# Optimization experiments

Measured on AMD Instinct MI355X. Metric: run time of the kernel, lower is better.

Reference implementation:

```python
import jax, jax.numpy as jnp
import numpy as np

N = 50000
E = 800000
IN_FEATS = 256
N_HIDDEN = 64
N_CLASSES = 40
HEADS = (4, 1)
NEG_SLOPE = 0.2  # DGL GATConv default


def gat_layer(x, src, dst, W, attn_l, attn_r, bias, n_heads, out_dim, activation):
    """One dglnn.GATConv layer (eval mode: dropout disabled).

    x: [N, F_in]; src/dst: [E] edge endpoints; W: [F_in, H*D];
    attn_l/attn_r: [H, D]; bias: [H*D]. Returns [N, H, D].
    """
    n = x.shape[0]
    z = (x @ W).reshape(n, n_heads, out_dim)            # [N, H, D]
    el = jnp.sum(z * attn_l[None], axis=-1)            # [N, H]
    er = jnp.sum(z * attn_r[None], axis=-1)            # [N, H]
    e = jax.nn.leaky_relu(el[src] + er[dst], NEG_SLOPE)  # [E, H]
    # segment softmax over incoming edges of each dst node
    m = jax.ops.segment_max(e, dst, num_segments=n)     # [N, H]
    a = jnp.exp(e - m[dst])                             # [E, H]
    s = jax.ops.segment_sum(a, dst, num_segments=n)     # [N, H]
    alpha = a / s[dst]                                  # [E, H]
    msg = alpha[:, :, None] * z[src]                    # [E, H, D]
    out = jax.ops.segment_sum(msg, dst, num_segments=n)  # [N, H, D]
    out = out + bias.reshape(1, n_heads, out_dim)
    if activation is not None:
        out = activation(out)
    return out


def setup_inputs() -> dict:
    key = jax.random.key(0)
    ks = jax.random.split(key, 12)
    H0, H1 = HEADS
    d_in1 = N_HIDDEN * H0
    def glorot(k, shape):
        fan = sum(shape[:2]) if len(shape) > 1 else shape[0]
        return jax.random.normal(k, shape, jnp.float32) * (2.0 / fan) ** 0.5
    return {
        "x": jax.random.normal(ks[0], (N, IN_FEATS), jnp.float32),
        "src": jax.random.randint(ks[1], (E,), 0, N),
        "dst": jax.random.randint(ks[2], (E,), 0, N),
        "W0": glorot(ks[3], (IN_FEATS, H0 * N_HIDDEN)),
        "attn_l0": glorot(ks[4], (H0, N_HIDDEN)),
        "attn_r0": glorot(ks[5], (H0, N_HIDDEN)),
        "bias0": jnp.zeros((H0 * N_HIDDEN,), jnp.float32),
        "W1": glorot(ks[6], (d_in1, H1 * N_CLASSES)),
        "attn_l1": glorot(ks[7], (H1, N_CLASSES)),
        "attn_r1": glorot(ks[8], (H1, N_CLASSES)),
        "bias1": jnp.zeros((H1 * N_CLASSES,), jnp.float32),
    }


def reference(x, src, dst, W0, attn_l0, attn_r0, bias0, W1, attn_l1, attn_r1, bias1):
    H0, H1 = HEADS
    # layer 0: GATConv + ELU, then flatten heads (l==0 branch)
    h = gat_layer(x, src, dst, W0, attn_l0, attn_r0, bias0,
                  H0, N_HIDDEN, jax.nn.elu)              # [N, H0, D]
    h = h.reshape(h.shape[0], -1)                        # [N, H0*D]
    # layer 1 (last): GATConv, no activation, head-mean (l==1 branch)
    h = gat_layer(h, src, dst, W1, attn_l1, attn_r1, bias1,
                  H1, N_CLASSES, None)                   # [N, H1, C]
    return h.mean(axis=1)                                # [N, C]
```

## Files before the change

kernel.cpp:

```cpp
#include <hip/hip_runtime.h>
#include <math.h>

using bf16x8 = __attribute__((ext_vector_type(8))) short;
using f32x4  = __attribute__((ext_vector_type(4))) float;

__device__ __forceinline__ unsigned short f2bf(float v) {
  unsigned int b = __float_as_uint(v);
  unsigned int r = (b + 0x7fffu + ((b >> 16) & 1u)) >> 16;
  return (unsigned short)r;
}
__device__ __forceinline__ float bf2f(unsigned short u) {
  return __uint_as_float(((unsigned int)u) << 16);
}


__global__ void mega0_kernel(const float* __restrict__ W0f, unsigned short* __restrict__ Bp0,
                             const float* __restrict__ W1f, unsigned short* __restrict__ Bp1,
                             const int* __restrict__ dst, int* __restrict__ deg, int E) {
  int bx = blockIdx.x;
  if (bx >= 38) {
    int t = (bx - 38) * 256 + threadIdx.x;
    if (t < E) atomicAdd(&deg[dst[t]], 1);
    return;
  }
  int idx = bx * 256 + threadIdx.x;
  if (idx < 8192) {
    int lane = idx & 63, s = (idx >> 6) & 7, t = idx >> 9;
    int n = t * 16 + (lane & 15), quad = lane >> 4;
    unsigned short* o = Bp0 + (size_t)idx * 8;
    #pragma unroll
    for (int j = 0; j < 8; ++j) {
      int k = s * 32 + quad * 8 + j;
      o[j] = f2bf(W0f[(size_t)k * 256 + n]);
    }
  } else if (idx < 8192 + 1536) {
    int i1 = idx - 8192;
    int lane = i1 & 63, s = (i1 >> 6) & 7, t = i1 >> 9;
    int n = t * 16 + (lane & 15), quad = lane >> 4;
    unsigned short* o = Bp1 + (size_t)i1 * 8;
    #pragma unroll
    for (int j = 0; j < 8; ++j) {
      int k = s * 32 + quad * 8 + j;
      o[j] = (n < 40) ? f2bf(W1f[(size_t)k * 40 + n]) : 0;
    }
  }
}


__global__ void block_sum_kernel(const int* __restrict__ deg, int* __restrict__ bsum, int n) {
  __shared__ int red[4];
  int t = threadIdx.x, i = blockIdx.x * 256 + t;
  int v = (i < n) ? deg[i] : 0;
  #pragma unroll
  for (int off = 32; off; off >>= 1) v += __shfl_xor(v, off);
  if ((t & 63) == 0) red[t >> 6] = v;
  __syncthreads();
  if (t == 0) bsum[blockIdx.x] = red[0] + red[1] + red[2] + red[3];
}

__global__ void scan_bsum_kernel(const int* __restrict__ bsum, int* __restrict__ boffs,
                                 int* __restrict__ offsets, int nb, int n) {
  __shared__ int tmp[1024];
  int t = threadIdx.x;
  int v = (t < nb) ? bsum[t] : 0;
  tmp[t] = v;
  __syncthreads();
  #pragma unroll
  for (int off = 1; off < 1024; off <<= 1) {
    int add = (t >= off) ? tmp[t - off] : 0;
    __syncthreads();
    tmp[t] += add;
    __syncthreads();
  }
  if (t < nb) boffs[t] = tmp[t] - v;
  if (t == 1023) offsets[n] = tmp[1023];
}

__global__ void write_offsets_kernel(const int* __restrict__ deg, const int* __restrict__ boffs,
                                     int* __restrict__ offsets, int* __restrict__ cursor, int n) {
  __shared__ int tmp[256];
  int t = threadIdx.x, i = blockIdx.x * 256 + t;
  int v = (i < n) ? deg[i] : 0;
  tmp[t] = v;
  __syncthreads();
  #pragma unroll
  for (int off = 1; off < 256; off <<= 1) {
    int add = (t >= off) ? tmp[t - off] : 0;
    __syncthreads();
    tmp[t] += add;
    __syncthreads();
  }
  if (i < n) {
    int o = boffs[blockIdx.x] + tmp[t] - v;
    offsets[i] = o;
    cursor[i] = o;
  }
}


__global__ __launch_bounds__(512) void mega2_kernel(
    const float* __restrict__ A, const unsigned short* __restrict__ Bp,
    unsigned short* __restrict__ Zb,
    const float* __restrict__ al, const float* __restrict__ arr,
    float* __restrict__ el, float* __restrict__ er, int M,
    const int* __restrict__ src, const int* __restrict__ dst,
    int* __restrict__ cursor, int* __restrict__ ssrc, int E, int nG, int nC) {
  __shared__ unsigned short Bs[32768];
  int bx = blockIdx.x;
  int tid = threadIdx.x;

  if (bx >= nG) {
    int stride = nC * 512;
    for (int e = (bx - nG) * 512 + tid; e < E; e += stride) {
      int p = atomicAdd(&cursor[dst[e]], 1);
      ssrc[p] = src[e];
    }
    return;
  }

  int gx = bx >> 1, y = bx & 1;
  {
    const int4* s4 = (const int4*)(Bp + (size_t)y * 32768);
    int4* d4 = (int4*)Bs;
    #pragma unroll
    for (int i = 0; i < 8; ++i) d4[tid + i * 512] = s4[tid + i * 512];
  }
  __syncthreads();

  int wid = tid >> 6, lane = tid & 63;
  int quad = lane >> 4, col16 = lane & 15;
  int wr = wid >> 1, wc = wid & 1;
  int rowbase = gx * 256 + wr * 64;

  const float* aptr[4];
  #pragma unroll
  for (int rt = 0; rt < 4; ++rt) {
    int m = rowbase + rt * 16 + col16;
    if (m > M - 1) m = M - 1;
    aptr[rt] = A + (size_t)m * 256 + quad * 8;
  }

  f32x4 acc[4][4];
  #pragma unroll
  for (int rt = 0; rt < 4; ++rt)
    #pragma unroll
    for (int ct = 0; ct < 4; ++ct) acc[rt][ct] = {0.f, 0.f, 0.f, 0.f};

  const bf16x8* BsV = (const bf16x8*)Bs;

  auto loadA = [&](bf16x8* fr, int s) {
    #pragma unroll
    for (int rt = 0; rt < 4; ++rt) {
      const float* ap = aptr[rt] + s * 32;
      float4 a0 = *(const float4*)ap;
      float4 a1 = *(const float4*)(ap + 4);
      fr[rt][0] = (short)f2bf(a0.x); fr[rt][1] = (short)f2bf(a0.y);
      fr[rt][2] = (short)f2bf(a0.z); fr[rt][3] = (short)f2bf(a0.w);
      fr[rt][4] = (short)f2bf(a1.x); fr[rt][5] = (short)f2bf(a1.y);
      fr[rt][6] = (short)f2bf(a1.z); fr[rt][7] = (short)f2bf(a1.w);
    }
  };

  bf16x8 afc[4];
  loadA(afc, 0);
  for (int s = 0; s < 8; ++s) {
    bf16x8 afn[4];
    if (s < 7) loadA(afn, s + 1);
    #pragma unroll
    for (int ct = 0; ct < 4; ++ct) {
      bf16x8 bf = BsV[((wc * 4 + ct) * 8 + s) * 64 + lane];
      #pragma unroll
      for (int rt = 0; rt < 4; ++rt)
        acc[rt][ct] = __builtin_amdgcn_mfma_f32_16x16x32_bf16(afc[rt], bf, acc[rt][ct], 0, 0, 0);
    }
    if (s < 7) {
      #pragma unroll
      for (int rt = 0; rt < 4; ++rt) afc[rt] = afn[rt];
    }
  }

  int hw = y * 2 + wc;
  float al_c[4], ar_c[4];
  #pragma unroll
  for (int ct = 0; ct < 4; ++ct) {
    int col = y * 128 + (wc * 4 + ct) * 16 + col16;
    al_c[ct] = al[col];
    ar_c[ct] = arr[col];
  }

  #pragma unroll
  for (int rt = 0; rt < 4; ++rt) {
    int row0 = rowbase + rt * 16 + quad * 4;
    #pragma unroll
    for (int r = 0; r < 4; ++r) {
      int row = row0 + r;
      if (row < M) {
        #pragma unroll
        for (int ct = 0; ct < 4; ++ct) {
          int col = y * 128 + (wc * 4 + ct) * 16 + col16;
          Zb[(size_t)row * 256 + col] = f2bf(acc[rt][ct][r]);
        }
      }
      float pe = 0.f, pr = 0.f;
      #pragma unroll
      for (int ct = 0; ct < 4; ++ct) {
        float zv = acc[rt][ct][r];
        pe += zv * al_c[ct];
        pr += zv * ar_c[ct];
      }
      pe += __shfl_xor(pe, 1); pr += __shfl_xor(pr, 1);
      pe += __shfl_xor(pe, 2); pr += __shfl_xor(pr, 2);
      pe += __shfl_xor(pe, 4); pr += __shfl_xor(pr, 4);
      pe += __shfl_xor(pe, 8); pr += __shfl_xor(pr, 8);
      if (col16 == 0 && row < M) {
        el[(size_t)row * 4 + hw] = pe;
        er[(size_t)row * 4 + hw] = pr;
      }
    }
  }
}


__global__ __launch_bounds__(256) void gemm1_mfma_kernel(
    const unsigned short* __restrict__ Ab, const unsigned short* __restrict__ Bp,
    unsigned short* __restrict__ Zb,
    const float* __restrict__ al, const float* __restrict__ arr,
    float* __restrict__ el, float* __restrict__ er, int M) {
  int wid = threadIdx.x >> 6, lane = threadIdx.x & 63;
  int quad = lane >> 4, col16 = lane & 15;
  int m = blockIdx.x * 64 + wid * 16 + col16;

  f32x4 acc[3];
  #pragma unroll
  for (int t = 0; t < 3; ++t) acc[t] = {0.f, 0.f, 0.f, 0.f};

  const bf16x8* BpV = (const bf16x8*)Bp;

  for (int s = 0; s < 8; ++s) {
    bf16x8 af;
    if (m < M) {
      af = *(const bf16x8*)(Ab + (size_t)m * 256 + s * 32 + quad * 8);
    } else {
      #pragma unroll
      for (int j = 0; j < 8; ++j) af[j] = 0;
    }
    #pragma unroll
    for (int t = 0; t < 3; ++t) {
      bf16x8 bf = BpV[(t * 8 + s) * 64 + lane];
      acc[t] = __builtin_amdgcn_mfma_f32_16x16x32_bf16(af, bf, acc[t], 0, 0, 0);
    }
  }

  float al_c[3], ar_c[3];
  #pragma unroll
  for (int t = 0; t < 3; ++t) {
    int col = t * 16 + col16;
    al_c[t] = (col < 40) ? al[col] : 0.f;
    ar_c[t] = (col < 40) ? arr[col] : 0.f;
  }

  int row0 = blockIdx.x * 64 + wid * 16 + quad * 4;
  #pragma unroll
  for (int r = 0; r < 4; ++r) {
    int row = row0 + r;
    if (row < M) {
      #pragma unroll
      for (int t = 0; t < 3; ++t) {
        int col = t * 16 + col16;
        if (col < 40) Zb[(size_t)row * 40 + col] = f2bf(acc[t][r]);
      }
    }
    float pe = 0.f, pr = 0.f;
    #pragma unroll
    for (int t = 0; t < 3; ++t) {
      pe += acc[t][r] * al_c[t];
      pr += acc[t][r] * ar_c[t];
    }
    pe += __shfl_xor(pe, 1); pr += __shfl_xor(pr, 1);
    pe += __shfl_xor(pe, 2); pr += __shfl_xor(pr, 2);
    pe += __shfl_xor(pe, 4); pr += __shfl_xor(pr, 4);
    pe += __shfl_xor(pe, 8); pr += __shfl_xor(pr, 8);
    if (col16 == 0 && row < M) {
      el[row] = pe;
      er[row] = pr;
    }
  }
}


__global__ __launch_bounds__(256) void agg0_kernel(
    const int* __restrict__ offs, const int* __restrict__ ssrc,
    const float* __restrict__ el, const float* __restrict__ er,
    const unsigned short* __restrict__ zb, const float* __restrict__ bias,
    unsigned short* __restrict__ outb, int n) {
  __shared__ float sW[4][16][4];
  __shared__ int   sS[4][16];
  int wid  = threadIdx.x >> 6;
  int lane = threadIdx.x & 63;
  int node = blockIdx.x * 4 + wid;
  if (node >= n) return;
  int c = lane & 3, eoff = lane >> 2;
  int half = lane >> 5, colg = lane & 31, h2 = colg >> 3;
  int s0 = offs[node], s1 = offs[node + 1];
  float er_c = er[node * 4 + c];

  float ssum = 0.f;
  float acc[8] = {0.f, 0.f, 0.f, 0.f, 0.f, 0.f, 0.f, 0.f};
  for (int base = s0; base < s1; base += 16) {
    int cnt = min(16, s1 - base);
    if (eoff < cnt) {
      int esrc = ssrc[base + eoff];
      float v = el[esrc * 4 + c] + er_c;
      v = v > 0.f ? v : 0.2f * v;
      sW[wid][eoff][c] = expf(v);
      if (c == 0) sS[wid][eoff] = esrc;
    }
    for (int j = 0; j < cnt; j += 2) {
      int jj = j + half;
      float w = (jj < cnt) ? sW[wid][jj][h2] : 0.f;
      int sn = sS[wid][(jj < cnt) ? jj : (cnt - 1)];
      ssum += w;
      bf16x8 zu = *(const bf16x8*)(zb + (size_t)sn * 256 + (colg << 3));
      #pragma unroll
      for (int i = 0; i < 8; ++i)
        acc[i] += w * bf2f((unsigned short)zu[i]);
    }
  }

  ssum += __shfl_xor(ssum, 32);
  #pragma unroll
  for (int i = 0; i < 8; ++i) acc[i] += __shfl_xor(acc[i], 32);

  float inv = (s1 > s0) ? 1.f / ssum : 0.f;
  if (half == 0) {
    const float4 b0v = *(const float4*)(bias + (colg << 3));
    const float4 b1v = *(const float4*)(bias + (colg << 3) + 4);
    float bb[8] = {b0v.x, b0v.y, b0v.z, b0v.w, b1v.x, b1v.y, b1v.z, b1v.w};
    bf16x8 u;
    #pragma unroll
    for (int i = 0; i < 8; ++i) {
      float o = acc[i] * inv + bb[i];
      o = o > 0.f ? o : expm1f(o);
      u[i] = (short)f2bf(o);
    }
    *(bf16x8*)(outb + (size_t)node * 256 + (colg << 3)) = u;
  }
}


__global__ __launch_bounds__(256) void agg1_kernel(
    const int* __restrict__ offs, const int* __restrict__ ssrc,
    const float* __restrict__ el, const float* __restrict__ er,
    const unsigned short* __restrict__ zb, const float* __restrict__ bias,
    float* __restrict__ out, int n) {
  __shared__ float sW[4][64];
  __shared__ int   sS[4][64];
  int wid  = threadIdx.x >> 6;
  int lane = threadIdx.x & 63;
  int node = blockIdx.x * 4 + wid;
  if (node >= n) return;
  int half = lane >> 5, d = lane & 31;
  int s0 = offs[node], s1 = offs[node + 1];
  float ern = er[node];

  float ssum = 0.f;
  float2 acc = make_float2(0.f, 0.f);
  for (int base = s0; base < s1; base += 64) {
    int cnt = min(64, s1 - base);
    if (lane < cnt) {
      int esrc = ssrc[base + lane];
      float v = el[esrc] + ern;
      v = v > 0.f ? v : 0.2f * v;
      sW[wid][lane] = expf(v);
      sS[wid][lane] = esrc;
    }
    for (int j = 0; j < cnt; j += 2) {
      int jj = j + half;
      float w = (jj < cnt) ? sW[wid][jj] : 0.f;
      int sn = sS[wid][(jj < cnt) ? jj : (cnt - 1)];
      ssum += w;
      if (d < 20) {
        unsigned zp = *(const unsigned*)(zb + (size_t)sn * 40 + (d << 1));
        acc.x += w * bf2f((unsigned short)(zp & 0xffffu));
        acc.y += w * bf2f((unsigned short)(zp >> 16));
      }
    }
  }

  ssum  += __shfl_xor(ssum, 32);
  acc.x += __shfl_xor(acc.x, 32);
  acc.y += __shfl_xor(acc.y, 32);

  float inv = (s1 > s0) ? 1.f / ssum : 0.f;
  if (half == 0 && d < 20) {
    float2 o;
    o.x = acc.x * inv + bias[(d << 1) + 0];
    o.y = acc.y * inv + bias[(d << 1) + 1];
    *(float2*)(out + (size_t)node * 40 + (d << 1)) = o;
  }
}


extern "C" void kernel_launch(void* const* d_in, const int* in_sizes, int n_in,
                              void* d_out, int out_size, void* d_ws, size_t ws_size,
                              hipStream_t stream) {
  const float* x   = (const float*)d_in[0];
  const int*   src = (const int*)d_in[1];
  const int*   dst = (const int*)d_in[2];
  const float* W0  = (const float*)d_in[3];
  const float* al0 = (const float*)d_in[4];
  const float* ar0 = (const float*)d_in[5];
  const float* b0  = (const float*)d_in[6];
  const float* W1  = (const float*)d_in[7];
  const float* al1 = (const float*)d_in[8];
  const float* ar1 = (const float*)d_in[9];
  const float* b1  = (const float*)d_in[10];
  float* out = (float*)d_out;

  const int N = in_sizes[0] / 256;
  const int E = in_sizes[1];
  const int NB = (N + 255) / 256;

  char* ws = (char*)d_ws;
  size_t off = 0;
  auto alloc = [&](size_t bytes) {
    void* p = ws + off;
    off = (off + bytes + 255) & ~(size_t)255;
    return p;
  };
  unsigned short* z0b = (unsigned short*)alloc((size_t)N * 256 * 2);
  unsigned short* h0b = (unsigned short*)alloc((size_t)N * 256 * 2);
  unsigned short* z1b = (unsigned short*)alloc((size_t)N * 40 * 2);
  unsigned short* w0p = (unsigned short*)alloc((size_t)16 * 8 * 64 * 8 * 2);
  unsigned short* w1p = (unsigned short*)alloc((size_t)3 * 8 * 64 * 8 * 2);
  float* el0  = (float*)alloc((size_t)N * 4 * 4);
  float* er0  = (float*)alloc((size_t)N * 4 * 4);
  float* el1  = (float*)alloc((size_t)N * 4);
  float* er1  = (float*)alloc((size_t)N * 4);
  int* deg    = (int*)alloc((size_t)N * 4);
  int* offs   = (int*)alloc((size_t)(N + 1) * 4);
  int* cursor = (int*)alloc((size_t)N * 4);
  int* bsum   = (int*)alloc((size_t)NB * 4);
  int* boffs  = (int*)alloc((size_t)NB * 4);
  int* ssrc   = (int*)alloc((size_t)E * 4);
  (void)off; (void)ws_size; (void)n_in; (void)out_size;

  const int nG = ((N + 255) / 256) * 2;
  const int nH = (E + 255) / 256;
  const int nC = 391;

  hipMemsetAsync(deg, 0, (size_t)N * 4, stream);
  mega0_kernel<<<38 + nH, 256, 0, stream>>>(W0, w0p, W1, w1p, dst, deg, E);
  block_sum_kernel<<<NB, 256, 0, stream>>>(deg, bsum, N);
  scan_bsum_kernel<<<1, 1024, 0, stream>>>(bsum, boffs, offs, NB, N);
  write_offsets_kernel<<<NB, 256, 0, stream>>>(deg, boffs, offs, cursor, N);
  mega2_kernel<<<nG + nC, 512, 0, stream>>>(x, w0p, z0b, al0, ar0, el0, er0, N,
                                            src, dst, cursor, ssrc, E, nG, nC);
  agg0_kernel<<<(N + 3) / 4, 256, 0, stream>>>(offs, ssrc, el0, er0, z0b, b0, h0b, N);
  gemm1_mfma_kernel<<<(N + 63) / 64, 256, 0, stream>>>(h0b, w1p, z1b, al1, ar1, el1, er1, N);
  agg1_kernel<<<(N + 3) / 4, 256, 0, stream>>>(offs, ssrc, el1, er1, z1b, b1, out, N);
}
```

Before: 318.0 us.

## Pre-convert x to bf16 in setup kernel and feed GEMM bf16 directly

Adds a bf16 conversion pass for x into the first setup kernel, writing into the h0b buffer, so the layer-0 GEMM reads half-width bf16 A tiles instead of converting fp32 on the fly. The GEMM also issues its first A load before staging the weights into LDS and fully unrolls the k loop. This adds an extra full read of x plus a write of its bf16 copy, in exchange for halving A traffic and removing conversion ALU work inside each of the two column-tile blocks that read the same rows. It relies on h0b not being used until agg0 overwrites it.

```diff
diff --git a/kernel.cpp b/kernel.cpp
--- a/kernel.cpp
+++ b/kernel.cpp
@@ -16,11 +16,27 @@
 
 __global__ void mega0_kernel(const float* __restrict__ W0f, unsigned short* __restrict__ Bp0,
                              const float* __restrict__ W1f, unsigned short* __restrict__ Bp1,
-                             const int* __restrict__ dst, int* __restrict__ deg, int E) {
+                             const float* __restrict__ xf, unsigned short* __restrict__ xb,
+                             const int* __restrict__ dst, int* __restrict__ deg,
+                             int E, int nCV, size_t NT) {
   int bx = blockIdx.x;
+  if (bx >= 38 + nCV) {
+    int t = (bx - 38 - nCV) * 256 + threadIdx.x;
+    if (t < E) atomicAdd(&deg[dst[t]], 1);
+    return;
+  }
   if (bx >= 38) {
-    int t = (bx - 38) * 256 + threadIdx.x;
-    if (t < E) atomicAdd(&deg[dst[t]], 1);
+    size_t i = ((size_t)(bx - 38) * 256 + threadIdx.x) * 8;
+    if (i + 8 <= NT) {
+      float4 a0 = *(const float4*)(xf + i);
+      float4 a1 = *(const float4*)(xf + i + 4);
+      bf16x8 u;
+      u[0] = (short)f2bf(a0.x); u[1] = (short)f2bf(a0.y);
+      u[2] = (short)f2bf(a0.z); u[3] = (short)f2bf(a0.w);
+      u[4] = (short)f2bf(a1.x); u[5] = (short)f2bf(a1.y);
+      u[6] = (short)f2bf(a1.z); u[7] = (short)f2bf(a1.w);
+      *(bf16x8*)(xb + i) = u;
+    }
     return;
   }
   int idx = bx * 256 + threadIdx.x;
@@ -99,7 +115,7 @@
 
 
 __global__ __launch_bounds__(512) void mega2_kernel(
-    const float* __restrict__ A, const unsigned short* __restrict__ Bp,
+    const unsigned short* __restrict__ Ab, const unsigned short* __restrict__ Bp,
     unsigned short* __restrict__ Zb,
     const float* __restrict__ al, const float* __restrict__ arr,
     float* __restrict__ el, float* __restrict__ er, int M,
@@ -119,50 +135,45 @@
   }
 
   int gx = bx >> 1, y = bx & 1;
-  {
-    const int4* s4 = (const int4*)(Bp + (size_t)y * 32768);
-    int4* d4 = (int4*)Bs;
-    #pragma unroll
-    for (int i = 0; i < 8; ++i) d4[tid + i * 512] = s4[tid + i * 512];
-  }
-  __syncthreads();
-
   int wid = tid >> 6, lane = tid & 63;
   int quad = lane >> 4, col16 = lane & 15;
   int wr = wid >> 1, wc = wid & 1;
   int rowbase = gx * 256 + wr * 64;
 
-  const float* aptr[4];
+  const unsigned short* aptr[4];
   #pragma unroll
   for (int rt = 0; rt < 4; ++rt) {
     int m = rowbase + rt * 16 + col16;
     if (m > M - 1) m = M - 1;
-    aptr[rt] = A + (size_t)m * 256 + quad * 8;
-  }
-
-  f32x4 acc[4][4];
-  #pragma unroll
-  for (int rt = 0; rt < 4; ++rt)
-    #pragma unroll
-    for (int ct = 0; ct < 4; ++ct) acc[rt][ct] = {0.f, 0.f, 0.f, 0.f};
-
-  const bf16x8* BsV = (const bf16x8*)Bs;
+    aptr[rt] = Ab + (size_t)m * 256 + quad * 8;
+  }
 
   auto loadA = [&](bf16x8* fr, int s) {
     #pragma unroll
-    for (int rt = 0; rt < 4; ++rt) {
-      const float* ap = aptr[rt] + s * 32;
-      float4 a0 = *(const float4*)ap;
-      float4 a1 = *(const float4*)(ap + 4);
-      fr[rt][0] = (short)f2bf(a0.x); fr[rt][1] = (short)f2bf(a0.y);
-      fr[rt][2] = (short)f2bf(a0.z); fr[rt][3] = (short)f2bf(a0.w);
-      fr[rt][4] = (short)f2bf(a1.x); fr[rt][5] = (short)f2bf(a1.y);
-      fr[rt][6] = (short)f2bf(a1.z); fr[rt][7] = (short)f2bf(a1.w);
-    }
+    for (int rt = 0; rt < 4; ++rt)
+      fr[rt] = *(const bf16x8*)(aptr[rt] + s * 32);
   };
 
   bf16x8 afc[4];
   loadA(afc, 0);
+
+  {
+    const int4* s4 = (const int4*)(Bp + (size_t)y * 32768);
+    int4* d4 = (int4*)Bs;
+    #pragma unroll
+    for (int i = 0; i < 8; ++i) d4[tid + i * 512] = s4[tid + i * 512];
+  }
+  __syncthreads();
+
+  f32x4 acc[4][4];
+  #pragma unroll
+  for (int rt = 0; rt < 4; ++rt)
+    #pragma unroll
+    for (int ct = 0; ct < 4; ++ct) acc[rt][ct] = {0.f, 0.f, 0.f, 0.f};
+
+  const bf16x8* BsV = (const bf16x8*)Bs;
+
+  #pragma unroll
   for (int s = 0; s < 8; ++s) {
     bf16x8 afn[4];
     if (s < 7) loadA(afn, s + 1);
@@ -445,16 +456,20 @@
   int* ssrc   = (int*)alloc((size_t)E * 4);
   (void)off; (void)ws_size; (void)n_in; (void)out_size;
 
+  unsigned short* xb = h0b;
+  const size_t NT = (size_t)N * 256;
+  const int nCV = (int)((NT / 8 + 255) / 256);
+
   const int nG = ((N + 255) / 256) * 2;
   const int nH = (E + 255) / 256;
   const int nC = 391;
 
   hipMemsetAsync(deg, 0, (size_t)N * 4, stream);
-  mega0_kernel<<<38 + nH, 256, 0, stream>>>(W0, w0p, W1, w1p, dst, deg, E);
+  mega0_kernel<<<38 + nCV + nH, 256, 0, stream>>>(W0, w0p, W1, w1p, x, xb, dst, deg, E, nCV, NT);
   block_sum_kernel<<<NB, 256, 0, stream>>>(deg, bsum, N);
   scan_bsum_kernel<<<1, 1024, 0, stream>>>(bsum, boffs, offs, NB, N);
   write_offsets_kernel<<<NB, 256, 0, stream>>>(deg, boffs, offs, cursor, N);
-  mega2_kernel<<<nG + nC, 512, 0, stream>>>(x, w0p, z0b, al0, ar0, el0, er0, N,
+  mega2_kernel<<<nG + nC, 512, 0, stream>>>(xb, w0p, z0b, al0, ar0, el0, er0, N,
                                             src, dst, cursor, ssrc, E, nG, nC);
   agg0_kernel<<<(N + 3) / 4, 256, 0, stream>>>(offs, ssrc, el0, er0, z0b, b0, h0b, N);
   gemm1_mfma_kernel<<<(N + 63) / 64, 256, 0, stream>>>(h0b, w1p, z1b, al1, ar1, el1, er1, N);
```

Result: slower. 327.7 us (+3.0%).
